# Kernel tuning notes

Measured on AMD Instinct MI355X. Metric: run time of the kernel, lower is better.

## Reference

```python
import jax, jax.numpy as jnp
import numpy as np

K = 100          # constructor k
CHUNK = 8192     # candidate dataset batch size
PENALTY = 1.0e5  # score penalty used by _exclude


def setup_inputs() -> dict:
    key = jax.random.key(0)
    kq, kc, ke = jax.random.split(key, 3)
    B, D, N, E = 512, 128, 1_048_576, 50
    queries = jax.random.normal(kq, (B, D), dtype=jnp.float32)
    candidates = jax.random.normal(kc, (N, D), dtype=jnp.float32)
    identifiers = jnp.arange(N, dtype=jnp.int32)
    exclusions = jax.random.randint(ke, (B, E), 0, N, dtype=jnp.int32)
    return {"queries": queries, "candidates": candidates,
            "identifiers": identifiers, "exclusions": exclusions}


def _streaming_topk(queries, candidates, identifiers, adj_k, chunk):
    """Streams candidate chunks, maintaining a running top-adj_k per query."""
    B = queries.shape[0]
    n_chunks = candidates.shape[0] // chunk
    cand = candidates.reshape(n_chunks, chunk, -1)          # [n_chunks, C, D]
    ids = identifiers.reshape(n_chunks, chunk)              # [n_chunks, C]

    init = (jnp.full((B, adj_k), -jnp.inf, queries.dtype),
            jnp.full((B, adj_k), -1, identifiers.dtype))

    def step(state, batch):
        s_scores, s_ids = state
        c, cid = batch
        # dot-product scoring: [B, C]
        scores = jnp.einsum('bd,cd->bc', queries, c)
        joined_s = jnp.concatenate([s_scores, scores], axis=1)
        joined_i = jnp.concatenate(
            [s_ids, jnp.broadcast_to(cid[None, :], (B, cid.shape[0]))], axis=1)
        top_s, idx = jax.lax.top_k(joined_s, adj_k)
        top_i = jnp.take_along_axis(joined_i, idx, axis=1)
        return (top_s, top_i), None

    (top_s, top_i), _ = jax.lax.scan(step, init, (cand, ids))
    return top_s, top_i


def reference(queries, candidates, identifiers, exclusions):
    E = exclusions.shape[1]
    adj_k = K + E  # query_with_exclusions: adjusted_k = k + num_exclusions
    scores, ids = _streaming_topk(queries, candidates, identifiers, adj_k, CHUNK)
    # _exclude: broadcast identifier equality mask, penalize, re-top-k
    isin = jnp.any(ids[:, :, None] == exclusions[:, None, :], axis=-1)
    adjusted = scores - isin.astype(scores.dtype) * PENALTY
    _, idx = jax.lax.top_k(adjusted, K)
    top_scores = jnp.take_along_axis(scores, idx, axis=1)
    top_ids = jnp.take_along_axis(ids, idx, axis=1)
    return top_scores, top_ids
```

## Files before the change

kernel.cpp:

```cpp
#include <hip/hip_runtime.h>
#include <cstdint>
#include <cfloat>

#define NQ     512
#define DIM    128
#define NCAND  1048576
#define TOPK   150
#define KOUT   100
#define NEXCL  50
#define STATE_STRIDE 160
#define POOL   2048

#define SEED_C   32768
#define SURV_CAP 16384
#define SCAN_QT  128
#define SCAN_CT  128

__global__ __launch_bounds__(256) void score_gemm(
    const float* __restrict__ q,
    const float* __restrict__ cand,
    float* __restrict__ S,
    int cand_base, int C)
{
  __shared__ float As[64 * 128];
  __shared__ float Bs[64 * 128];
  const int t  = threadIdx.x;
  const int c0 = blockIdx.x * 64;
  const int q0 = blockIdx.y * 64;

  for (int iter = 0; iter < 8; ++iter) {
    int idx = iter * 256 + t;
    int row = idx >> 5;
    int c4  = idx & 31;
    int sw  = c4 ^ ((row >> 2) & 7);
    float4 av = *(const float4*)(q + (size_t)(q0 + row) * DIM + c4 * 4);
    *(float4*)(As + row * 128 + sw * 4) = av;
    float4 bv = *(const float4*)(cand + (size_t)(cand_base + c0 + row) * DIM + c4 * 4);
    *(float4*)(Bs + row * 128 + sw * 4) = bv;
  }
  __syncthreads();

  const int tm = t >> 4;
  const int tn = t & 15;
  float acc[4][4];
#pragma unroll
  for (int m = 0; m < 4; ++m)
#pragma unroll
    for (int n = 0; n < 4; ++n) acc[m][n] = 0.0f;

#pragma unroll 4
  for (int k4 = 0; k4 < 32; ++k4) {
    float4 a[4], b[4];
#pragma unroll
    for (int m = 0; m < 4; ++m)
      a[m] = *(const float4*)(As + (4 * tm + m) * 128 + ((k4 ^ (tm & 7)) * 4));
#pragma unroll
    for (int n = 0; n < 4; ++n)
      b[n] = *(const float4*)(Bs + (4 * tn + n) * 128 + ((k4 ^ (tn & 7)) * 4));
#pragma unroll
    for (int m = 0; m < 4; ++m)
#pragma unroll
      for (int n = 0; n < 4; ++n) {
        acc[m][n] += a[m].x * b[n].x;
        acc[m][n] += a[m].y * b[n].y;
        acc[m][n] += a[m].z * b[n].z;
        acc[m][n] += a[m].w * b[n].w;
      }
  }

#pragma unroll
  for (int m = 0; m < 4; ++m) {
    float4 v = make_float4(acc[m][0], acc[m][1], acc[m][2], acc[m][3]);
    *(float4*)(S + (size_t)(q0 + 4 * tm + m) * C + c0 + 4 * tn) = v;
  }
}

__device__ inline void bitonic_sort_desc(float* ps, int* pi, int t)
{
  for (int size = 2; size <= POOL; size <<= 1) {
    for (int stride = size >> 1; stride > 0; stride >>= 1) {
      __syncthreads();
      for (int i = t; i < POOL / 2; i += 256) {
        int idx = 2 * i - (i & (stride - 1));
        int j   = idx + stride;
        bool desc = ((idx & size) == 0);
        float s1 = ps[idx], s2 = ps[j];
        int   i1 = pi[idx], i2 = pi[j];
        bool jBetter = (s2 > s1) || (s2 == s1 && i2 < i1);
        if (jBetter == desc) {
          ps[idx] = s2; ps[j] = s1;
          pi[idx] = i2; pi[j] = i1;
        }
      }
    }
  }
  __syncthreads();
}

__global__ __launch_bounds__(256) void topk_merge(
    const float* __restrict__ S,
    float* __restrict__ st_s,
    int*   __restrict__ st_i,
    int*   __restrict__ cnts,
    int cand_base, int C, int first)
{
  __shared__ float ps[POOL];
  __shared__ int   pi[POOL];
  __shared__ int   cnt;
  __shared__ float thr;
  const int b = blockIdx.x;
  const int t = threadIdx.x;

  if (t == 0) {
    cnt = first ? 0 : TOPK;
    thr = first ? -FLT_MAX : st_s[(size_t)b * STATE_STRIDE + TOPK - 1];
    if (first) cnts[b] = 0;
  }
  if (!first && t < TOPK) {
    ps[t] = st_s[(size_t)b * STATE_STRIDE + t];
    pi[t] = st_i[(size_t)b * STATE_STRIDE + t];
  }
  __syncthreads();

  const float4* row = (const float4*)(S + (size_t)b * C);
  const int nIter = C >> 10;
  for (int it = 0; it < nIter; ++it) {
    if (cnt + 1024 > POOL) {
      int c = cnt;
      for (int i = t; i < POOL; i += 256)
        if (i >= c) { ps[i] = -FLT_MAX; pi[i] = 0x7fffffff; }
      __syncthreads();
      bitonic_sort_desc(ps, pi, t);
      if (t == 0) { cnt = (c < TOPK) ? c : TOPK; thr = ps[TOPK - 1]; }
      __syncthreads();
    }
    float4 v = row[it * 256 + t];
    int base_id = cand_base + it * 1024 + t * 4;
    float sv[4] = {v.x, v.y, v.z, v.w};
#pragma unroll
    for (int jj = 0; jj < 4; ++jj) {
      if (sv[jj] >= thr) {
        int p = atomicAdd(&cnt, 1);
        ps[p] = sv[jj];
        pi[p] = base_id + jj;
      }
    }
    __syncthreads();
  }

  {
    int c = cnt;
    for (int i = t; i < POOL; i += 256)
      if (i >= c) { ps[i] = -FLT_MAX; pi[i] = 0x7fffffff; }
    __syncthreads();
    bitonic_sort_desc(ps, pi, t);
  }
  if (t < TOPK) {
    st_s[(size_t)b * STATE_STRIDE + t] = ps[t];
    st_i[(size_t)b * STATE_STRIDE + t] = pi[t];
  }
}

__global__ __launch_bounds__(256, 2) void scan_filter(
    const float* __restrict__ q,
    const float* __restrict__ cand,
    const float* __restrict__ st_s,
    float2* __restrict__ surv,
    int*    __restrict__ cnts,
    int cand_base)
{
  __shared__ float As[SCAN_QT * 64];
  __shared__ float Bs[SCAN_CT * 64];
  __shared__ float thr_s[SCAN_QT];

  const int t  = threadIdx.x;
  const int q0 = blockIdx.x * SCAN_QT;
  const int cb = cand_base + blockIdx.y * SCAN_CT;
  const int tm = t >> 4;
  const int tn = t & 15;

  if (t < SCAN_QT)
    thr_s[t] = st_s[(size_t)(q0 + t) * STATE_STRIDE + (TOPK - 1)];

  float acc[8][8];
#pragma unroll
  for (int m = 0; m < 8; ++m)
#pragma unroll
    for (int n = 0; n < 8; ++n) acc[m][n] = 0.0f;

  const int swa = tm & 7, swb = tn & 7;

  for (int h = 0; h < 2; ++h) {
    __syncthreads();
    for (int iter = 0; iter < 8; ++iter) {
      int idx = iter * 256 + t;
      int row = idx >> 4;
      int c4  = idx & 15;
      int sw  = c4 ^ ((row >> 3) & 7);
      float4 av = *(const float4*)(q + (size_t)(q0 + row) * DIM + h * 64 + c4 * 4);
      *(float4*)(As + row * 64 + sw * 4) = av;
      float4 bv = *(const float4*)(cand + (size_t)(cb + row) * DIM + h * 64 + c4 * 4);
      *(float4*)(Bs + row * 64 + sw * 4) = bv;
    }
    __syncthreads();

#pragma unroll 4
    for (int k4 = 0; k4 < 16; ++k4) {
      float4 a[8], b[8];
      const int ca = (k4 ^ swa) * 4;
      const int cbx = (k4 ^ swb) * 4;
#pragma unroll
      for (int m = 0; m < 8; ++m)
        a[m] = *(const float4*)(As + (8 * tm + m) * 64 + ca);
#pragma unroll
      for (int n = 0; n < 8; ++n)
        b[n] = *(const float4*)(Bs + (8 * tn + n) * 64 + cbx);
#pragma unroll
      for (int m = 0; m < 8; ++m)
#pragma unroll
        for (int n = 0; n < 8; ++n) {
          acc[m][n] += a[m].x * b[n].x;
          acc[m][n] += a[m].y * b[n].y;
          acc[m][n] += a[m].z * b[n].z;
          acc[m][n] += a[m].w * b[n].w;
        }
    }
  }

#pragma unroll
  for (int m = 0; m < 8; ++m) {
    const float th = thr_s[8 * tm + m];
    const int   qg = q0 + 8 * tm + m;
#pragma unroll
    for (int n = 0; n < 8; ++n) {
      if (acc[m][n] >= th) {
        int p = atomicAdd(&cnts[qg], 1);
        if (p < SURV_CAP)
          surv[(size_t)qg * SURV_CAP + p] =
              make_float2(acc[m][n], __int_as_float(cb + 8 * tn + n));
      }
    }
  }
}

__global__ __launch_bounds__(256) void topk_final(
    const float2* __restrict__ surv,
    const int*    __restrict__ cnts,
    float* __restrict__ st_s,
    int*   __restrict__ st_i)
{
  __shared__ float ps[POOL];
  __shared__ int   pi[POOL];
  __shared__ int   cnt;
  __shared__ float thr;
  const int b = blockIdx.x;
  const int t = threadIdx.x;

  if (t == 0) {
    cnt = TOPK;
    thr = st_s[(size_t)b * STATE_STRIDE + TOPK - 1];
  }
  if (t < TOPK) {
    ps[t] = st_s[(size_t)b * STATE_STRIDE + t];
    pi[t] = st_i[(size_t)b * STATE_STRIDE + t];
  }
  __syncthreads();

  int n = cnts[b];
  if (n > SURV_CAP) n = SURV_CAP;
  const float2* row = surv + (size_t)b * SURV_CAP;

  for (int base = 0; base < n; base += 1024) {
    if (cnt + 1024 > POOL) {
      int c = cnt;
      for (int i = t; i < POOL; i += 256)
        if (i >= c) { ps[i] = -FLT_MAX; pi[i] = 0x7fffffff; }
      __syncthreads();
      bitonic_sort_desc(ps, pi, t);
      if (t == 0) { cnt = (c < TOPK) ? c : TOPK; thr = ps[TOPK - 1]; }
      __syncthreads();
    }
#pragma unroll
    for (int jj = 0; jj < 4; ++jj) {
      int i = base + jj * 256 + t;
      if (i < n) {
        float2 e = row[i];
        if (e.x >= thr) {
          int p = atomicAdd(&cnt, 1);
          ps[p] = e.x;
          pi[p] = __float_as_int(e.y);
        }
      }
    }
    __syncthreads();
  }

  {
    int c = cnt;
    for (int i = t; i < POOL; i += 256)
      if (i >= c) { ps[i] = -FLT_MAX; pi[i] = 0x7fffffff; }
    __syncthreads();
    bitonic_sort_desc(ps, pi, t);
  }
  if (t < TOPK) {
    st_s[(size_t)b * STATE_STRIDE + t] = ps[t];
    st_i[(size_t)b * STATE_STRIDE + t] = pi[t];
  }
}

__global__ __launch_bounds__(256) void finalize(
    const float* __restrict__ st_s,
    const int*   __restrict__ st_i,
    const int*   __restrict__ excl,
    float* __restrict__ out)
{
  const int b = blockIdx.x;
  const int t = threadIdx.x;
  __shared__ int ex[NEXCL];
  __shared__ unsigned char keep[TOPK];
  __shared__ short pos[TOPK];

  if (t < NEXCL) ex[t] = excl[(size_t)b * NEXCL + t];
  __syncthreads();
  if (t < TOPK) {
    int id = st_i[(size_t)b * STATE_STRIDE + t];
    bool k = true;
#pragma unroll
    for (int j = 0; j < NEXCL; ++j) k = k && (id != ex[j]);
    keep[t] = (unsigned char)k;
  }
  __syncthreads();
  if (t == 0) {
    int p = 0;
    for (int i = 0; i < TOPK; ++i) {
      pos[i] = (keep[i] && p < KOUT) ? (short)p : (short)-1;
      if (keep[i]) ++p;
    }
  }
  __syncthreads();
  if (t < TOPK) {
    int p = pos[t];
    if (p >= 0) {
      out[(size_t)b * KOUT + p] = st_s[(size_t)b * STATE_STRIDE + t];
      out[(size_t)NQ * KOUT + (size_t)b * KOUT + p] =
          (float)st_i[(size_t)b * STATE_STRIDE + t];
    }
  }
}

extern "C" void kernel_launch(void* const* d_in, const int* in_sizes, int n_in,
                              void* d_out, int out_size, void* d_ws, size_t ws_size,
                              hipStream_t stream)
{
  (void)in_sizes; (void)n_in; (void)out_size; (void)ws_size;
  const float* q    = (const float*)d_in[0];
  const float* cand = (const float*)d_in[1];
  const int*   excl = (const int*)d_in[3];
  float* out = (float*)d_out;

  const size_t state_one = (size_t)NQ * STATE_STRIDE * 4;
  float*  st_s = (float*)d_ws;
  int*    st_i = (int*)((char*)d_ws + state_one);
  int*    cnts = (int*)((char*)d_ws + 2 * state_one);
  float*  S    = (float*)((char*)d_ws + 2 * state_one + 4096);
  float2* surv = (float2*)((char*)d_ws + 2 * state_one + 4096 +
                           (size_t)NQ * SEED_C * 4);

  dim3 g1(SEED_C / 64, NQ / 64);
  score_gemm<<<g1, 256, 0, stream>>>(q, cand, S, 0, SEED_C);
  topk_merge<<<NQ, 256, 0, stream>>>(S, st_s, st_i, cnts, 0, SEED_C, 1);

  dim3 g2(NQ / SCAN_QT, (NCAND - SEED_C) / SCAN_CT);
  scan_filter<<<g2, 256, 0, stream>>>(q, cand, st_s, surv, cnts, SEED_C);

  topk_final<<<NQ, 256, 0, stream>>>(surv, cnts, st_s, st_i);
  finalize<<<NQ, 256, 0, stream>>>(st_s, st_i, excl, out);
}
```

Before: 2.807 ms.

## Restructure scan_filter to read candidates once and broadcast transposed queries via scalar loads

```diff
diff --git a/kernel.cpp b/kernel.cpp
--- a/kernel.cpp
+++ b/kernel.cpp
@@ -13,8 +13,16 @@
 
 #define SEED_C   32768
 #define SURV_CAP 16384
-#define SCAN_QT  128
 #define SCAN_CT  128
+
+__global__ __launch_bounds__(256) void transpose_q(
+    const float* __restrict__ q, float* __restrict__ qt)
+{
+  int idx = blockIdx.x * 256 + threadIdx.x;
+  int qi = idx >> 7;
+  int k  = idx & 127;
+  qt[(size_t)k * NQ + qi] = q[(size_t)qi * DIM + k];
+}
 
 __global__ __launch_bounds__(256) void score_gemm(
     const float* __restrict__ q,
@@ -161,83 +169,70 @@
   }
 }
 
-__global__ __launch_bounds__(256, 2) void scan_filter(
-    const float* __restrict__ q,
+__global__ __launch_bounds__(256, 4) void scan_filter(
+    const float* __restrict__ qt,
     const float* __restrict__ cand,
     const float* __restrict__ st_s,
     float2* __restrict__ surv,
     int*    __restrict__ cnts,
     int cand_base)
 {
-  __shared__ float As[SCAN_QT * 64];
-  __shared__ float Bs[SCAN_CT * 64];
-  __shared__ float thr_s[SCAN_QT];
-
+  __shared__ float Bs[64 * SCAN_CT];
   const int t  = threadIdx.x;
-  const int q0 = blockIdx.x * SCAN_QT;
-  const int cb = cand_base + blockIdx.y * SCAN_CT;
-  const int tm = t >> 4;
-  const int tn = t & 15;
-
-  if (t < SCAN_QT)
-    thr_s[t] = st_s[(size_t)(q0 + t) * STATE_STRIDE + (TOPK - 1)];
-
-  float acc[8][8];
-#pragma unroll
-  for (int m = 0; m < 8; ++m)
-#pragma unroll
-    for (int n = 0; n < 8; ++n) acc[m][n] = 0.0f;
-
-  const int swa = tm & 7, swb = tn & 7;
-
-  for (int h = 0; h < 2; ++h) {
-    __syncthreads();
-    for (int iter = 0; iter < 8; ++iter) {
-      int idx = iter * 256 + t;
-      int row = idx >> 4;
-      int c4  = idx & 15;
-      int sw  = c4 ^ ((row >> 3) & 7);
-      float4 av = *(const float4*)(q + (size_t)(q0 + row) * DIM + h * 64 + c4 * 4);
-      *(float4*)(As + row * 64 + sw * 4) = av;
-      float4 bv = *(const float4*)(cand + (size_t)(cb + row) * DIM + h * 64 + c4 * 4);
-      *(float4*)(Bs + row * 64 + sw * 4) = bv;
-    }
-    __syncthreads();
-
+  const int l  = t & 63;
+  const int w  = t >> 6;
+  const int cb = cand_base + blockIdx.x * SCAN_CT;
+
+  const int sr = t & 127;
+  const int sc = (t >> 7) * 8;
+  const float* myrow = cand + (size_t)(cb + sr) * DIM;
+
+  for (int qb = 0; qb < 4; ++qb) {
+    const int qw = __builtin_amdgcn_readfirstlane(qb * 128 + w * 32);
+
+    float acc[32][2];
+#pragma unroll
+    for (int i = 0; i < 32; ++i) { acc[i][0] = 0.0f; acc[i][1] = 0.0f; }
+
+    for (int h = 0; h < 2; ++h) {
+      __syncthreads();
+#pragma unroll
+      for (int cc = 0; cc < 8; ++cc) {
+        int c4 = sc + cc;
+        float4 v = *(const float4*)(myrow + h * 64 + 4 * c4);
+        Bs[(4 * c4 + 0) * SCAN_CT + sr] = v.x;
+        Bs[(4 * c4 + 1) * SCAN_CT + sr] = v.y;
+        Bs[(4 * c4 + 2) * SCAN_CT + sr] = v.z;
+        Bs[(4 * c4 + 3) * SCAN_CT + sr] = v.w;
+      }
+      __syncthreads();
+
+      const float* aw = qt + (size_t)(h * 64) * NQ + qw;
 #pragma unroll 4
-    for (int k4 = 0; k4 < 16; ++k4) {
-      float4 a[8], b[8];
-      const int ca = (k4 ^ swa) * 4;
-      const int cbx = (k4 ^ swb) * 4;
-#pragma unroll
-      for (int m = 0; m < 8; ++m)
-        a[m] = *(const float4*)(As + (8 * tm + m) * 64 + ca);
-#pragma unroll
-      for (int n = 0; n < 8; ++n)
-        b[n] = *(const float4*)(Bs + (8 * tn + n) * 64 + cbx);
-#pragma unroll
-      for (int m = 0; m < 8; ++m)
-#pragma unroll
-        for (int n = 0; n < 8; ++n) {
-          acc[m][n] += a[m].x * b[n].x;
-          acc[m][n] += a[m].y * b[n].y;
-          acc[m][n] += a[m].z * b[n].z;
-          acc[m][n] += a[m].w * b[n].w;
+      for (int kk = 0; kk < 64; ++kk) {
+        float b0 = Bs[kk * SCAN_CT + l];
+        float b1 = Bs[kk * SCAN_CT + l + 64];
+#pragma unroll
+        for (int i = 0; i < 32; ++i) {
+          float a = aw[(size_t)kk * NQ + i];
+          acc[i][0] = fmaf(a, b0, acc[i][0]);
+          acc[i][1] = fmaf(a, b1, acc[i][1]);
         }
-    }
-  }
-
-#pragma unroll
-  for (int m = 0; m < 8; ++m) {
-    const float th = thr_s[8 * tm + m];
-    const int   qg = q0 + 8 * tm + m;
-#pragma unroll
-    for (int n = 0; n < 8; ++n) {
-      if (acc[m][n] >= th) {
-        int p = atomicAdd(&cnts[qg], 1);
-        if (p < SURV_CAP)
-          surv[(size_t)qg * SURV_CAP + p] =
-              make_float2(acc[m][n], __int_as_float(cb + 8 * tn + n));
+      }
+    }
+
+#pragma unroll
+    for (int i = 0; i < 32; ++i) {
+      const int   qg = qw + i;
+      const float th = st_s[(size_t)qg * STATE_STRIDE + (TOPK - 1)];
+#pragma unroll
+      for (int j = 0; j < 2; ++j) {
+        if (acc[i][j] >= th) {
+          int p = atomicAdd(&cnts[qg], 1);
+          if (p < SURV_CAP)
+            surv[(size_t)qg * SURV_CAP + p] =
+                make_float2(acc[i][j], __int_as_float(cb + l + 64 * j));
+        }
       }
     }
   }
@@ -365,13 +360,16 @@
   float*  S    = (float*)((char*)d_ws + 2 * state_one + 4096);
   float2* surv = (float2*)((char*)d_ws + 2 * state_one + 4096 +
                            (size_t)NQ * SEED_C * 4);
+  float*  qt   = (float*)((char*)surv + (size_t)NQ * SURV_CAP * 8);
+
+  transpose_q<<<NQ * DIM / 256, 256, 0, stream>>>(q, qt);
 
   dim3 g1(SEED_C / 64, NQ / 64);
   score_gemm<<<g1, 256, 0, stream>>>(q, cand, S, 0, SEED_C);
   topk_merge<<<NQ, 256, 0, stream>>>(S, st_s, st_i, cnts, 0, SEED_C, 1);
 
-  dim3 g2(NQ / SCAN_QT, (NCAND - SEED_C) / SCAN_CT);
-  scan_filter<<<g2, 256, 0, stream>>>(q, cand, st_s, surv, cnts, SEED_C);
+  scan_filter<<<(NCAND - SEED_C) / SCAN_CT, 256, 0, stream>>>(
+      qt, cand, st_s, surv, cnts, SEED_C);
 
   topk_final<<<NQ, 256, 0, stream>>>(surv, cnts, st_s, st_i);
   finalize<<<NQ, 256, 0, stream>>>(st_s, st_i, excl, out);
```

Result: slower. 4.496 ms (+60.2%).
